# Optimization experiments

Measured on AMD Instinct MI355X. Metric: run time of the kernel, lower is better.

## Reference

```python
import jax, jax.numpy as jnp
import numpy as np

# Loss hyperparameters (from init_kwargs defaults)
ALPHA, BETA, GAMMA = 1.0, 2.0, 1.0
DAY_W, NIGHT_W = 2.0, 0.5
PEAK_WIN_W, PEAK_WIN = 3.0, 2
HIGH_POWER_W, POWER_PCT = 1.5, 0.75
HOURS = 24

B, S = 4096, 4032  # seq_len = 24 * 168 days


def setup_inputs() -> dict:
    key = jax.random.key(0)
    k1, k2 = jax.random.split(key)
    y_true = jax.random.uniform(k1, (B, S), dtype=jnp.float32)
    # predictions = truth + noise, clipped to be realistic power values
    y_pred = y_true + 0.1 * jax.random.normal(k2, (B, S), dtype=jnp.float32)
    return {"y_pred": y_pred, "y_true": y_true}


def _daily_peaks(y, day_mask):
    # y, day_mask: (B, D, H). Peaks restricted to daytime hours.
    masked = jnp.where(day_mask, y, jnp.float32(-1e9))
    times = jnp.argmax(masked, axis=-1)                                   # (B, D) int
    vals = jnp.take_along_axis(y, times[..., None], axis=-1)[..., 0]      # (B, D)
    return times, vals


def reference(y_pred, y_true):
    b, s = y_true.shape
    d = s // HOURS
    # default is_daytime: hour-of-day in [6, 20]
    hour = jnp.arange(HOURS, dtype=jnp.int32)
    day_hour_mask = (hour >= 6) & (hour <= 20)                            # (H,)
    is_daytime = jnp.broadcast_to(day_hour_mask[None, None, :], (b, d, HOURS))

    yt = y_true.reshape(b, d, HOURS)
    yp = y_pred.reshape(b, d, HOURS)

    true_times, true_peaks = _daily_peaks(yt, is_daytime)
    pred_times, pred_peaks = _daily_peaks(yp, is_daytime)
    peak_time_errors = (pred_times - true_times).astype(jnp.float32)      # (B, D)

    # --- step weights: day/night base, x PEAK_WIN_W in [peak-2, peak+2] ---
    base_w = jnp.where(is_daytime, jnp.float32(DAY_W), jnp.float32(NIGHT_W))  # (B,D,H)
    pt = true_times[..., None]                                            # (B,D,1)
    in_window = (hour[None, None, :] >= pt - PEAK_WIN) & (hour[None, None, :] <= pt + PEAK_WIN)
    step_w = base_w * jnp.where(in_window, jnp.float32(PEAK_WIN_W), jnp.float32(1.0))
    step_w = step_w.reshape(b, s)

    sq_err = (y_pred - y_true) ** 2
    L_overall = jnp.sum(sq_err * step_w) / jnp.sum(step_w)

    # --- peak magnitude loss with high-power sample weighting ---
    sample_avg_peaks = jnp.mean(true_peaks, axis=1)                       # (B,)
    thr = jnp.quantile(sample_avg_peaks, POWER_PCT)
    high = sample_avg_peaks > thr                                         # (B,) bool
    sample_w = jnp.where(high[:, None], jnp.float32(HIGH_POWER_W), jnp.float32(1.0))
    sample_w = jnp.broadcast_to(sample_w, true_peaks.shape)               # (B, D)
    peak_sq = (pred_peaks - true_peaks) ** 2
    L_peak_mag = jnp.sum(peak_sq * sample_w) / jnp.sum(sample_w)

    L_peak_timing = jnp.mean(jnp.abs(peak_time_errors) * 10.0)

    return ALPHA * L_overall + BETA * L_peak_mag + GAMMA * L_peak_timing
```

## Files before the change

kernel.cpp:

```cpp
#include <hip/hip_runtime.h>
#include <math.h>

#define HOURS   24
#define DPS     168
#define S_LEN   4032
#define NB_MAX  4096


__global__ __launch_bounds__(256) void day_kernel(
    const float* __restrict__ yTrue, const float* __restrict__ yPred,
    float* __restrict__ Aday, float* __restrict__ Pday,
    float* __restrict__ SEb, float* __restrict__ SWb, float* __restrict__ Tb,
    long long totalDays)
{
    __shared__ float s_red[3][4];
    const int tid = threadIdx.x;
    const int lane = tid & 63;
    const int wv = tid >> 6;

    const long long d = (long long)blockIdx.x * 256 + tid;
    const bool valid = d < totalDays;
    const long long dc = valid ? d : 0;

    const float4* gt = (const float4*)(yTrue + dc * HOURS);
    const float4* gp = (const float4*)(yPred + dc * HOURS);

    float4 t0 = gt[0], t1 = gt[1], t2 = gt[2], t3 = gt[3], t4 = gt[4], t5 = gt[5];
    float4 p0 = gp[0], p1 = gp[1], p2 = gp[2], p3 = gp[3], p4 = gp[4], p5 = gp[5];

    float yt[24], yp[24];
    yt[0]=t0.x; yt[1]=t0.y; yt[2]=t0.z; yt[3]=t0.w;
    yt[4]=t1.x; yt[5]=t1.y; yt[6]=t1.z; yt[7]=t1.w;
    yt[8]=t2.x; yt[9]=t2.y; yt[10]=t2.z; yt[11]=t2.w;
    yt[12]=t3.x; yt[13]=t3.y; yt[14]=t3.z; yt[15]=t3.w;
    yt[16]=t4.x; yt[17]=t4.y; yt[18]=t4.z; yt[19]=t4.w;
    yt[20]=t5.x; yt[21]=t5.y; yt[22]=t5.z; yt[23]=t5.w;
    yp[0]=p0.x; yp[1]=p0.y; yp[2]=p0.z; yp[3]=p0.w;
    yp[4]=p1.x; yp[5]=p1.y; yp[6]=p1.z; yp[7]=p1.w;
    yp[8]=p2.x; yp[9]=p2.y; yp[10]=p2.z; yp[11]=p2.w;
    yp[12]=p3.x; yp[13]=p3.y; yp[14]=p3.z; yp[15]=p3.w;
    yp[16]=p4.x; yp[17]=p4.y; yp[18]=p4.z; yp[19]=p4.w;
    yp[20]=p5.x; yp[21]=p5.y; yp[22]=p5.z; yp[23]=p5.w;

    float tbest = yt[6]; int tt = 6;
#pragma unroll
    for (int h = 7; h <= 20; ++h) if (yt[h] > tbest) { tbest = yt[h]; tt = h; }
    float pbest = yp[6]; int pt = 6;
#pragma unroll
    for (int h = 7; h <= 20; ++h) if (yp[h] > pbest) { pbest = yp[h]; pt = h; }

    float se = 0.f, sw = 0.f;
#pragma unroll
    for (int h = 0; h < 24; ++h) {
        float bw = ((h >= 6) && (h <= 20)) ? 2.0f : 0.5f;
        float wgt = bw * (((h >= tt - 2) && (h <= tt + 2)) ? 3.0f : 1.0f);
        float dd = yp[h] - yt[h];
        se = fmaf(wgt * dd, dd, se);
        sw += wgt;
    }
    float te = fabsf((float)(pt - tt));
    if (!valid) { se = 0.f; sw = 0.f; te = 0.f; }

    if (valid) {
        Aday[d] = tbest;
        float dpk = pbest - tbest;
        Pday[d] = dpk * dpk;
    }

#pragma unroll
    for (int o = 32; o > 0; o >>= 1) {
        se += __shfl_down(se, o, 64);
        sw += __shfl_down(sw, o, 64);
        te += __shfl_down(te, o, 64);
    }
    if (lane == 0) { s_red[0][wv] = se; s_red[1][wv] = sw; s_red[2][wv] = te; }
    __syncthreads();
    if (tid == 0) {
        SEb[blockIdx.x] = s_red[0][0] + s_red[0][1] + s_red[0][2] + s_red[0][3];
        SWb[blockIdx.x] = s_red[1][0] + s_red[1][1] + s_red[1][2] + s_red[1][3];
        Tb[blockIdx.x]  = s_red[2][0] + s_red[2][1] + s_red[2][2] + s_red[2][3];
    }
}


__global__ __launch_bounds__(64) void sample_kernel(
    const float* __restrict__ Aday, const float* __restrict__ Pday,
    float* __restrict__ A, float* __restrict__ P)
{
    const int b = blockIdx.x;
    const int lane = threadIdx.x;
    const float* ad = Aday + (size_t)b * DPS;
    const float* pd = Pday + (size_t)b * DPS;
    float sa = 0.f, sp = 0.f;
    for (int i = lane; i < DPS; i += 64) { sa += ad[i]; sp += pd[i]; }
#pragma unroll
    for (int o = 32; o > 0; o >>= 1) {
        sa += __shfl_down(sa, o, 64);
        sp += __shfl_down(sp, o, 64);
    }
    if (lane == 0) { A[b] = sa * (1.0f / (float)DPS); P[b] = sp; }
}


__global__ __launch_bounds__(256) void rank_kernel(
    const float* __restrict__ A, float* __restrict__ qout, int nB)
{
    __shared__ float sA[NB_MAX];
    const int tid = threadIdx.x;

    for (int i = tid; i < nB; i += 256) sA[i] = A[i];
    __syncthreads();

    const int b = blockIdx.x * 64 + (tid >> 2);
    const int quar = tid & 3;
    if (b >= nB) return;
    const float v = sA[b];
    const int span = nB / 4;
    const float4* s4 = (const float4*)(sA + quar * span);

    int cl = 0, ce = 0;
    for (int i = 0; i < span / 4; ++i) {
        float4 x = s4[i];
        cl += (x.x < v) + (x.y < v) + (x.z < v) + (x.w < v);
        ce += (x.x == v) + (x.y == v) + (x.z == v) + (x.w == v);
    }
    cl += __shfl_xor(cl, 1, 64); ce += __shfl_xor(ce, 1, 64);
    cl += __shfl_xor(cl, 2, 64); ce += __shfl_xor(ce, 2, 64);

    if (quar == 0) {
        double pos = 0.75 * (double)(nB - 1);
        int lo = (int)pos;
        int hi = (lo + 1 < nB) ? lo + 1 : lo;
        if (lo >= cl && lo < cl + ce) qout[0] = v;
        if (hi >= cl && hi < cl + ce) qout[1] = v;
    }
}


__device__ inline double block_reduce_d(double v, double* scratch, int tid) {
#pragma unroll
    for (int o = 32; o > 0; o >>= 1) v += __shfl_down(v, o, 64);
    if ((tid & 63) == 0) scratch[tid >> 6] = v;
    __syncthreads();
    double r = 0.0;
    if (tid == 0) r = scratch[0] + scratch[1] + scratch[2] + scratch[3];
    __syncthreads();
    return r;
}

__global__ __launch_bounds__(256) void final_kernel(
    const float* __restrict__ SEb, const float* __restrict__ SWb,
    const float* __restrict__ Tb, const float* __restrict__ P,
    const float* __restrict__ A, const float* __restrict__ qout,
    float* __restrict__ out, int nB, int nBlk)
{
    __shared__ double s_dred[4];
    const int tid = threadIdx.x;

    double pos = 0.75 * (double)(nB - 1);
    double frac = pos - (double)((int)pos);
    float thr = (float)((double)qout[0] + frac * ((double)qout[1] - (double)qout[0]));

    double se = 0.0, sw = 0.0, te = 0.0, wp = 0.0, wsum = 0.0;
    for (int i = tid; i < nBlk; i += 256) {
        se += (double)SEb[i];
        sw += (double)SWb[i];
        te += (double)Tb[i];
    }
    for (int b = tid; b < nB; b += 256) {
        float w = (A[b] > thr) ? 1.5f : 1.0f;
        wp   += (double)w * (double)P[b];
        wsum += (double)w;
    }
    se   = block_reduce_d(se,   s_dred, tid);
    sw   = block_reduce_d(sw,   s_dred, tid);
    te   = block_reduce_d(te,   s_dred, tid);
    wp   = block_reduce_d(wp,   s_dred, tid);
    wsum = block_reduce_d(wsum, s_dred, tid);

    if (tid == 0) {
        double L_overall = se / sw;
        double L_peak    = wp / ((double)DPS * wsum);
        double L_timing  = 10.0 * te / ((double)nB * (double)DPS);
        out[0] = (float)(L_overall + 2.0 * L_peak + L_timing);
    }
}


extern "C" void kernel_launch(void* const* d_in, const int* in_sizes, int n_in,
                              void* d_out, int out_size, void* d_ws, size_t ws_size,
                              hipStream_t stream) {
    const float* y_pred = (const float*)d_in[0];
    const float* y_true = (const float*)d_in[1];
    int total = in_sizes[0];
    int nB = total / S_LEN;
    long long totalDays = (long long)nB * DPS;
    int nBlk = (int)((totalDays + 255) / 256);

    float* ws   = (float*)d_ws;
    float* Aday = ws;
    float* Pday = Aday + (size_t)totalDays;
    float* SEb  = Pday + (size_t)totalDays;
    float* SWb  = SEb + (size_t)nBlk;
    float* Tb   = SWb + (size_t)nBlk;
    float* A    = Tb  + (size_t)nBlk;
    float* P    = A   + (size_t)nB;
    float* q    = P   + (size_t)nB;

    day_kernel<<<nBlk, 256, 0, stream>>>(y_true, y_pred, Aday, Pday, SEb, SWb, Tb, totalDays);
    sample_kernel<<<nB, 64, 0, stream>>>(Aday, Pday, A, P);
    rank_kernel<<<(nB + 63) / 64, 256, 0, stream>>>(A, q, nB);
    final_kernel<<<1, 256, 0, stream>>>(SEb, SWb, Tb, P, A, q, (float*)d_out, nB, nBlk);
}
```

Before: 169.7 us.

## Fuse per-sample reduction into day kernel using block-per-3-samples layout

Restructures the day kernel so each 512-thread block handles three full samples (504 days) and reduces per-sample average peak and peak error in shared memory. This removes the separate sample_kernel launch and the global round trip for per-day Aday/Pday arrays. In exchange, 8 of the 512 threads per block sit idle and the block size doubles, which may affect occupancy.

```diff
diff --git a/kernel.cpp b/kernel.cpp
--- a/kernel.cpp
+++ b/kernel.cpp
@@ -4,26 +4,33 @@
 #define HOURS   24
 #define DPS     168
 #define S_LEN   4032
+#define SPB     3
 #define NB_MAX  4096
 
 
-__global__ __launch_bounds__(256) void day_kernel(
+__global__ __launch_bounds__(512) void day_kernel(
     const float* __restrict__ yTrue, const float* __restrict__ yPred,
-    float* __restrict__ Aday, float* __restrict__ Pday,
+    float* __restrict__ A, float* __restrict__ P,
     float* __restrict__ SEb, float* __restrict__ SWb, float* __restrict__ Tb,
-    long long totalDays)
+    int nB)
 {
-    __shared__ float s_red[3][4];
+    __shared__ float s_a[SPB * DPS + 8];
+    __shared__ float s_p[SPB * DPS + 8];
+    __shared__ float s_red[3][8];
+
     const int tid = threadIdx.x;
     const int lane = tid & 63;
     const int wv = tid >> 6;
 
-    const long long d = (long long)blockIdx.x * 256 + tid;
-    const bool valid = d < totalDays;
-    const long long dc = valid ? d : 0;
-
-    const float4* gt = (const float4*)(yTrue + dc * HOURS);
-    const float4* gp = (const float4*)(yPred + dc * HOURS);
+    const int s  = tid / DPS;
+    const int ds = tid - s * DPS;
+    const int b  = blockIdx.x * SPB + s;
+    const bool valid = (tid < SPB * DPS) && (b < nB);
+
+    const long long d = valid ? ((long long)b * DPS + ds) : 0;
+
+    const float4* gt = (const float4*)(yTrue + d * HOURS);
+    const float4* gp = (const float4*)(yPred + d * HOURS);
 
     float4 t0 = gt[0], t1 = gt[1], t2 = gt[2], t3 = gt[3], t4 = gt[4], t5 = gt[5];
     float4 p0 = gp[0], p1 = gp[1], p2 = gp[2], p3 = gp[3], p4 = gp[4], p5 = gp[5];
@@ -61,10 +68,10 @@
     float te = fabsf((float)(pt - tt));
     if (!valid) { se = 0.f; sw = 0.f; te = 0.f; }
 
-    if (valid) {
-        Aday[d] = tbest;
+    if (tid < SPB * DPS) {
         float dpk = pbest - tbest;
-        Pday[d] = dpk * dpk;
+        s_a[tid] = valid ? tbest : 0.f;
+        s_p[tid] = valid ? dpk * dpk : 0.f;
     }
 
 #pragma unroll
@@ -75,30 +82,31 @@
     }
     if (lane == 0) { s_red[0][wv] = se; s_red[1][wv] = sw; s_red[2][wv] = te; }
     __syncthreads();
+
     if (tid == 0) {
-        SEb[blockIdx.x] = s_red[0][0] + s_red[0][1] + s_red[0][2] + s_red[0][3];
-        SWb[blockIdx.x] = s_red[1][0] + s_red[1][1] + s_red[1][2] + s_red[1][3];
-        Tb[blockIdx.x]  = s_red[2][0] + s_red[2][1] + s_red[2][2] + s_red[2][3];
-    }
-}
-
-
-__global__ __launch_bounds__(64) void sample_kernel(
-    const float* __restrict__ Aday, const float* __restrict__ Pday,
-    float* __restrict__ A, float* __restrict__ P)
-{
-    const int b = blockIdx.x;
-    const int lane = threadIdx.x;
-    const float* ad = Aday + (size_t)b * DPS;
-    const float* pd = Pday + (size_t)b * DPS;
-    float sa = 0.f, sp = 0.f;
-    for (int i = lane; i < DPS; i += 64) { sa += ad[i]; sp += pd[i]; }
-#pragma unroll
-    for (int o = 32; o > 0; o >>= 1) {
-        sa += __shfl_down(sa, o, 64);
-        sp += __shfl_down(sp, o, 64);
-    }
-    if (lane == 0) { A[b] = sa * (1.0f / (float)DPS); P[b] = sp; }
+        float e = 0.f, w = 0.f, t = 0.f;
+#pragma unroll
+        for (int k = 0; k < 8; ++k) { e += s_red[0][k]; w += s_red[1][k]; t += s_red[2][k]; }
+        SEb[blockIdx.x] = e; SWb[blockIdx.x] = w; Tb[blockIdx.x] = t;
+    }
+
+    if (wv < SPB) {
+        const int bb = blockIdx.x * SPB + wv;
+        const float* sa = s_a + wv * DPS;
+        const float* sp = s_p + wv * DPS;
+        float a = sa[lane] + sa[lane + 64];
+        float p = sp[lane] + sp[lane + 64];
+        if (lane < DPS - 128) { a += sa[lane + 128]; p += sp[lane + 128]; }
+#pragma unroll
+        for (int o = 32; o > 0; o >>= 1) {
+            a += __shfl_down(a, o, 64);
+            p += __shfl_down(p, o, 64);
+        }
+        if (lane == 0 && bb < nB) {
+            A[bb] = a * (1.0f / (float)DPS);
+            P[bb] = p;
+        }
+    }
 }
 
 
@@ -194,21 +202,17 @@
     const float* y_true = (const float*)d_in[1];
     int total = in_sizes[0];
     int nB = total / S_LEN;
-    long long totalDays = (long long)nB * DPS;
-    int nBlk = (int)((totalDays + 255) / 256);
-
-    float* ws   = (float*)d_ws;
-    float* Aday = ws;
-    float* Pday = Aday + (size_t)totalDays;
-    float* SEb  = Pday + (size_t)totalDays;
-    float* SWb  = SEb + (size_t)nBlk;
-    float* Tb   = SWb + (size_t)nBlk;
-    float* A    = Tb  + (size_t)nBlk;
-    float* P    = A   + (size_t)nB;
-    float* q    = P   + (size_t)nB;
-
-    day_kernel<<<nBlk, 256, 0, stream>>>(y_true, y_pred, Aday, Pday, SEb, SWb, Tb, totalDays);
-    sample_kernel<<<nB, 64, 0, stream>>>(Aday, Pday, A, P);
+    int nBlk = (nB + SPB - 1) / SPB;
+
+    float* ws  = (float*)d_ws;
+    float* A   = ws;
+    float* P   = A   + (size_t)nB;
+    float* SEb = P   + (size_t)nB;
+    float* SWb = SEb + (size_t)nBlk;
+    float* Tb  = SWb + (size_t)nBlk;
+    float* q   = Tb  + (size_t)nBlk;
+
+    day_kernel<<<nBlk, 512, 0, stream>>>(y_true, y_pred, A, P, SEb, SWb, Tb, nB);
     rank_kernel<<<(nB + 63) / 64, 256, 0, stream>>>(A, q, nB);
     final_kernel<<<1, 256, 0, stream>>>(SEb, SWb, Tb, P, A, q, (float*)d_out, nB, nBlk);
 }
```

Result: faster. 164.3 us (-3.2%).
